# Kernel optimization log

Measured on AMD Instinct MI355X. Metric: run time of the kernel, lower is better.

The kernel has to match this reference:

```python
import jax, jax.numpy as jnp
import numpy as np

B, F, D = 1024, 16, 64
P = F * (F - 1) // 2  # 120 field pairs


def setup_inputs() -> dict:
    key = jax.random.key(0)
    k1, k2, k3 = jax.random.split(key, 3)
    x = jax.random.normal(k1, (B, F, D), dtype=jnp.float32)
    # torch Linear weight layout: [out_features, in_features] = [D, D*D], one per pair
    W = jax.random.normal(k2, (P, D, D * D), dtype=jnp.float32) * (1.0 / np.sqrt(D * D))
    b = jax.random.normal(k3, (P, D), dtype=jnp.float32) * 0.01
    return {"x": x, "W": W, "b": b}


def reference(x, W, b):
    # x: [B, F, D]; W: [P, D, D*D]; b: [P, D]
    Bs, Fs, Ds = x.shape
    Ps = W.shape[0]
    ii, jj = np.triu_indices(Fs, k=1)  # pair order matches nested (i, j>i) loop
    xi = x[:, ii, :]  # [B, P, D] -> left vector of outer product
    xj = x[:, jj, :]  # [B, P, D] -> right vector
    # Flattened outer tmp[b, a*D + c] = xi[b,p,a] * xj[b,p,c];
    # Linear: out = tmp @ W^T + b. Reshape W to [P, D_out, a, c] and fuse,
    # never materializing the [B, P, D*D] outer-product tensor.
    W3 = W.reshape(Ps, Ds, Ds, Ds)
    out = jnp.einsum('bpa,bpc,pkac->bpk', xi, xj, W3) + b[None, :, :]
    return out  # [B, P, D]
```

## Files before the change

kernel.cpp:

```cpp
#include <hip/hip_runtime.h>
#include <stdint.h>
#include <stddef.h>

constexpr int NB = 1024;
constexpr int NF = 16;
constexpr int ND = 64;
constexpr int NP = 120;
constexpr int KD = ND * ND;
constexpr int OUT_STRIDE = NP * ND;

using floatx4 = __attribute__((ext_vector_type(4))) float;
using short8  = __attribute__((ext_vector_type(8))) short;
using uint4v  = __attribute__((ext_vector_type(4))) uint32_t;

constexpr int XI_STRIDE = 68;
constexpr int BT_STRIDE = 72;

__device__ __forceinline__ uint32_t pack_bf16(float f0, float f1) {
    uint32_t u0 = __float_as_uint(f0) + 0x8000u;
    uint32_t u1 = __float_as_uint(f1) + 0x8000u;
    return __builtin_amdgcn_perm(u1, u0, 0x07060302u);
}

__global__ __launch_bounds__(256, 2)
void outer_kernel(const float* __restrict__ x, const float* __restrict__ W,
                  const float* __restrict__ bias, float* __restrict__ out)
{
    __shared__ float    lds_xi[256 * XI_STRIDE];
    __shared__ uint16_t lds_bt[ND * BT_STRIDE];

    const int p  = blockIdx.x;
    const int b0 = blockIdx.y * 256;

    int icol = 0, rem = p;
    while (rem >= NF - 1 - icol) { rem -= NF - 1 - icol; ++icol; }
    const int jcol = icol + 1 + rem;

    const int t    = threadIdx.x;
    const int wave = t >> 6;
    const int lane = t & 63;
    const int r    = lane & 15;
    const int quad = lane >> 4;

    {
        const float* src = x + (size_t)(b0 + t) * (NF * ND) + icol * ND;
        float* dst = lds_xi + t * XI_STRIDE;
        #pragma unroll
        for (int c = 0; c < ND; c += 4)
            *(floatx4*)(dst + c) = *(const floatx4*)(src + c);
    }

    float xj[4][2][8];
    #pragma unroll
    for (int ms = 0; ms < 4; ++ms) {
        const float* srow = x + (size_t)(b0 + wave*64 + ms*16 + r) * (NF * ND)
                              + jcol * ND + quad * 8;
        #pragma unroll
        for (int ks = 0; ks < 2; ++ks) {
            floatx4 v0 = *(const floatx4*)(srow + ks * 32);
            floatx4 v1 = *(const floatx4*)(srow + ks * 32 + 4);
            xj[ms][ks][0] = v0.x; xj[ms][ks][1] = v0.y;
            xj[ms][ks][2] = v0.z; xj[ms][ks][3] = v0.w;
            xj[ms][ks][4] = v1.x; xj[ms][ks][5] = v1.y;
            xj[ms][ks][6] = v1.z; xj[ms][ks][7] = v1.w;
        }
    }

    const int n_st = t >> 2;
    const int c_st = (t & 3) * 16;
    const float* wsrc = W + ((size_t)p * ND + n_st) * KD + c_st;
    uint16_t* bdst = lds_bt + n_st * BT_STRIDE + c_st;

    floatx4 w0 = *(const floatx4*)(wsrc + 0);
    floatx4 w1 = *(const floatx4*)(wsrc + 4);
    floatx4 w2 = *(const floatx4*)(wsrc + 8);
    floatx4 w3 = *(const floatx4*)(wsrc + 12);

    floatx4 acc[4][4] = {};

    #pragma unroll 1
    for (int a = 0; a < ND; ++a) {
        uint4v q0 = (uint4v){ pack_bf16(w0.x, w0.y), pack_bf16(w0.z, w0.w),
                              pack_bf16(w1.x, w1.y), pack_bf16(w1.z, w1.w) };
        uint4v q1 = (uint4v){ pack_bf16(w2.x, w2.y), pack_bf16(w2.z, w2.w),
                              pack_bf16(w3.x, w3.y), pack_bf16(w3.z, w3.w) };
        *(uint4v*)(bdst)     = q0;
        *(uint4v*)(bdst + 8) = q1;
        __syncthreads();

        if (a + 1 < ND) {
            const float* wn = wsrc + (size_t)(a + 1) * ND;
            w0 = *(const floatx4*)(wn + 0);
            w1 = *(const floatx4*)(wn + 4);
            w2 = *(const floatx4*)(wn + 8);
            w3 = *(const floatx4*)(wn + 12);
        }

        float xis[4];
        #pragma unroll
        for (int ms = 0; ms < 4; ++ms)
            xis[ms] = lds_xi[(wave*64 + ms*16 + r) * XI_STRIDE + a];

        #pragma unroll
        for (int ks = 0; ks < 2; ++ks) {
            short8 bf[4];
            #pragma unroll
            for (int ns = 0; ns < 4; ++ns)
                bf[ns] = *(const short8*)&lds_bt[(ns*16 + r) * BT_STRIDE
                                                 + ks*32 + quad*8];
            #pragma unroll
            for (int ms = 0; ms < 4; ++ms) {
                union { short8 s; uint32_t u[4]; } af;
                #pragma unroll
                for (int jj = 0; jj < 4; ++jj)
                    af.u[jj] = pack_bf16(xis[ms] * xj[ms][ks][2*jj],
                                         xis[ms] * xj[ms][ks][2*jj + 1]);
                #pragma unroll
                for (int ns = 0; ns < 4; ++ns)
                    acc[ms][ns] = __builtin_amdgcn_mfma_f32_16x16x32_bf16(
                        af.s, bf[ns], acc[ms][ns], 0, 0, 0);
            }
        }
        __syncthreads();
    }

    #pragma unroll
    for (int ns = 0; ns < 4; ++ns) {
        const float bb = bias[p * ND + ns*16 + r];
        #pragma unroll
        for (int ms = 0; ms < 4; ++ms) {
            #pragma unroll
            for (int reg = 0; reg < 4; ++reg) {
                const int row = b0 + wave*64 + ms*16 + quad*4 + reg;
                out[(size_t)row * OUT_STRIDE + p * ND + ns*16 + r]
                    = acc[ms][ns][reg] + bb;
            }
        }
    }
}

extern "C" void kernel_launch(void* const* d_in, const int* in_sizes, int n_in,
                              void* d_out, int out_size, void* d_ws, size_t ws_size,
                              hipStream_t stream) {
    const float* x    = (const float*)d_in[0];
    const float* W    = (const float*)d_in[1];
    const float* bias = (const float*)d_in[2];
    float* out = (float*)d_out;

    dim3 grid(NP, NB / 256);
    outer_kernel<<<grid, 256, 0, stream>>>(x, W, bias, out);
}
```

Measured before the change: 230.2 us.

## Factor xi scaling out of MFMA and double-buffer weight tiles in LDS

The kernel now keeps a fixed bf16 A fragment built from xj and runs MFMA against each weight slice with a zero accumulator. It then scales the result rows by xi[a] on the VALU and adds them into the accumulators, so the per-iteration xi*xj multiply and repack of A fragments goes away. xi is stored transposed in LDS as bf16, and the weight slice LDS buffer is double-buffered, which removes one barrier per iteration and prefetches two slices ahead. The cost is 64 extra VALU FMAs per iteration plus bf16 rounding of xi, and the separate per-a accumulation changes the numerics.

After: 379.1 us. +64.7%, slower.

```diff
diff --git a/kernel.cpp b/kernel.cpp
--- a/kernel.cpp
+++ b/kernel.cpp
@@ -12,8 +12,9 @@
 using floatx4 = __attribute__((ext_vector_type(4))) float;
 using short8  = __attribute__((ext_vector_type(8))) short;
 using uint4v  = __attribute__((ext_vector_type(4))) uint32_t;
+using ushort4v = __attribute__((ext_vector_type(4))) uint16_t;
 
-constexpr int XI_STRIDE = 68;
+constexpr int XT_STRIDE = 264;
 constexpr int BT_STRIDE = 72;
 
 __device__ __forceinline__ uint32_t pack_bf16(float f0, float f1) {
@@ -22,12 +23,20 @@
     return __builtin_amdgcn_perm(u1, u0, 0x07060302u);
 }
 
+__device__ __forceinline__ uint16_t to_bf16(float f) {
+    return (uint16_t)((__float_as_uint(f) + 0x8000u) >> 16);
+}
+
+__device__ __forceinline__ float from_bf16(uint16_t u) {
+    return __uint_as_float(((uint32_t)u) << 16);
+}
+
 __global__ __launch_bounds__(256, 2)
 void outer_kernel(const float* __restrict__ x, const float* __restrict__ W,
                   const float* __restrict__ bias, float* __restrict__ out)
 {
-    __shared__ float    lds_xi[256 * XI_STRIDE];
-    __shared__ uint16_t lds_bt[ND * BT_STRIDE];
+    __shared__ uint16_t lds_xit[ND * XT_STRIDE];
+    __shared__ uint16_t lds_bt[2][ND * BT_STRIDE];
 
     const int p  = blockIdx.x;
     const int b0 = blockIdx.y * 256;
@@ -44,13 +53,17 @@
 
     {
         const float* src = x + (size_t)(b0 + t) * (NF * ND) + icol * ND;
-        float* dst = lds_xi + t * XI_STRIDE;
         #pragma unroll
-        for (int c = 0; c < ND; c += 4)
-            *(floatx4*)(dst + c) = *(const floatx4*)(src + c);
+        for (int c = 0; c < ND; c += 4) {
+            floatx4 v = *(const floatx4*)(src + c);
+            lds_xit[(c + 0) * XT_STRIDE + t] = to_bf16(v.x);
+            lds_xit[(c + 1) * XT_STRIDE + t] = to_bf16(v.y);
+            lds_xit[(c + 2) * XT_STRIDE + t] = to_bf16(v.z);
+            lds_xit[(c + 3) * XT_STRIDE + t] = to_bf16(v.w);
+        }
     }
 
-    float xj[4][2][8];
+    short8 afrag[4][2];
     #pragma unroll
     for (int ms = 0; ms < 4; ++ms) {
         const float* srow = x + (size_t)(b0 + wave*64 + ms*16 + r) * (NF * ND)
@@ -59,68 +72,94 @@
         for (int ks = 0; ks < 2; ++ks) {
             floatx4 v0 = *(const floatx4*)(srow + ks * 32);
             floatx4 v1 = *(const floatx4*)(srow + ks * 32 + 4);
-            xj[ms][ks][0] = v0.x; xj[ms][ks][1] = v0.y;
-            xj[ms][ks][2] = v0.z; xj[ms][ks][3] = v0.w;
-            xj[ms][ks][4] = v1.x; xj[ms][ks][5] = v1.y;
-            xj[ms][ks][6] = v1.z; xj[ms][ks][7] = v1.w;
+            union { short8 s; uint32_t u[4]; } af;
+            af.u[0] = pack_bf16(v0.x, v0.y);
+            af.u[1] = pack_bf16(v0.z, v0.w);
+            af.u[2] = pack_bf16(v1.x, v1.y);
+            af.u[3] = pack_bf16(v1.z, v1.w);
+            afrag[ms][ks] = af.s;
         }
     }
 
     const int n_st = t >> 2;
     const int c_st = (t & 3) * 16;
     const float* wsrc = W + ((size_t)p * ND + n_st) * KD + c_st;
-    uint16_t* bdst = lds_bt + n_st * BT_STRIDE + c_st;
+    uint16_t* bdst0 = &lds_bt[0][n_st * BT_STRIDE + c_st];
+    uint16_t* bdst1 = &lds_bt[1][n_st * BT_STRIDE + c_st];
 
-    floatx4 w0 = *(const floatx4*)(wsrc + 0);
-    floatx4 w1 = *(const floatx4*)(wsrc + 4);
-    floatx4 w2 = *(const floatx4*)(wsrc + 8);
-    floatx4 w3 = *(const floatx4*)(wsrc + 12);
+    floatx4 wreg[2][4];
+
+    #pragma unroll
+    for (int q = 0; q < 4; ++q) wreg[0][q] = *(const floatx4*)(wsrc + q * 4);
+    {
+        uint4v q0 = (uint4v){ pack_bf16(wreg[0][0].x, wreg[0][0].y), pack_bf16(wreg[0][0].z, wreg[0][0].w),
+                              pack_bf16(wreg[0][1].x, wreg[0][1].y), pack_bf16(wreg[0][1].z, wreg[0][1].w) };
+        uint4v q1 = (uint4v){ pack_bf16(wreg[0][2].x, wreg[0][2].y), pack_bf16(wreg[0][2].z, wreg[0][2].w),
+                              pack_bf16(wreg[0][3].x, wreg[0][3].y), pack_bf16(wreg[0][3].z, wreg[0][3].w) };
+        *(uint4v*)(bdst0)     = q0;
+        *(uint4v*)(bdst0 + 8) = q1;
+    }
+    #pragma unroll
+    for (int q = 0; q < 4; ++q) wreg[1][q] = *(const floatx4*)(wsrc + ND + q * 4);
+    __syncthreads();
 
     floatx4 acc[4][4] = {};
+    const floatx4 zerof = (floatx4){0.f, 0.f, 0.f, 0.f};
 
-    #pragma unroll 1
+    #pragma unroll 2
     for (int a = 0; a < ND; ++a) {
-        uint4v q0 = (uint4v){ pack_bf16(w0.x, w0.y), pack_bf16(w0.z, w0.w),
-                              pack_bf16(w1.x, w1.y), pack_bf16(w1.z, w1.w) };
-        uint4v q1 = (uint4v){ pack_bf16(w2.x, w2.y), pack_bf16(w2.z, w2.w),
-                              pack_bf16(w3.x, w3.y), pack_bf16(w3.z, w3.w) };
-        *(uint4v*)(bdst)     = q0;
-        *(uint4v*)(bdst + 8) = q1;
-        __syncthreads();
+        const int cur = a & 1;
+
+        if (a + 2 < ND) {
+            const float* wn = wsrc + (size_t)(a + 2) * ND;
+            #pragma unroll
+            for (int q = 0; q < 4; ++q) wreg[cur][q] = *(const floatx4*)(wn + q * 4);
+        }
+
+        short8 bf[4][2];
+        #pragma unroll
+        for (int ns = 0; ns < 4; ++ns)
+            #pragma unroll
+            for (int ks = 0; ks < 2; ++ks)
+                bf[ns][ks] = *(const short8*)&lds_bt[cur][(ns*16 + r) * BT_STRIDE
+                                                          + ks*32 + quad*8];
+
+        float xiv[4][4];
+        #pragma unroll
+        for (int ms = 0; ms < 4; ++ms) {
+            ushort4v xv = *(const ushort4v*)&lds_xit[a * XT_STRIDE
+                                                     + wave*64 + ms*16 + quad*4];
+            xiv[ms][0] = from_bf16(xv.x);
+            xiv[ms][1] = from_bf16(xv.y);
+            xiv[ms][2] = from_bf16(xv.z);
+            xiv[ms][3] = from_bf16(xv.w);
+        }
+
+        #pragma unroll
+        for (int ms = 0; ms < 4; ++ms) {
+            #pragma unroll
+            for (int ns = 0; ns < 4; ++ns) {
+                floatx4 tacc = __builtin_amdgcn_mfma_f32_16x16x32_bf16(
+                    afrag[ms][0], bf[ns][0], zerof, 0, 0, 0);
+                tacc = __builtin_amdgcn_mfma_f32_16x16x32_bf16(
+                    afrag[ms][1], bf[ns][1], tacc, 0, 0, 0);
+                #pragma unroll
+                for (int reg = 0; reg < 4; ++reg)
+                    acc[ms][ns][reg] += xiv[ms][reg] * tacc[reg];
+            }
+        }
 
         if (a + 1 < ND) {
-            const float* wn = wsrc + (size_t)(a + 1) * ND;
-            w0 = *(const floatx4*)(wn + 0);
-            w1 = *(const floatx4*)(wn + 4);
-            w2 = *(const floatx4*)(wn + 8);
-            w3 = *(const floatx4*)(wn + 12);
+            const floatx4* wr = wreg[1 - cur];
+            uint4v q0 = (uint4v){ pack_bf16(wr[0].x, wr[0].y), pack_bf16(wr[0].z, wr[0].w),
+                                  pack_bf16(wr[1].x, wr[1].y), pack_bf16(wr[1].z, wr[1].w) };
+            uint4v q1 = (uint4v){ pack_bf16(wr[2].x, wr[2].y), pack_bf16(wr[2].z, wr[2].w),
+                                  pack_bf16(wr[3].x, wr[3].y), pack_bf16(wr[3].z, wr[3].w) };
+            uint16_t* bd = (cur ? bdst0 : bdst1);
+            *(uint4v*)(bd)     = q0;
+            *(uint4v*)(bd + 8) = q1;
         }
 
-        float xis[4];
-        #pragma unroll
-        for (int ms = 0; ms < 4; ++ms)
-            xis[ms] = lds_xi[(wave*64 + ms*16 + r) * XI_STRIDE + a];
-
-        #pragma unroll
-        for (int ks = 0; ks < 2; ++ks) {
-            short8 bf[4];
-            #pragma unroll
-            for (int ns = 0; ns < 4; ++ns)
-                bf[ns] = *(const short8*)&lds_bt[(ns*16 + r) * BT_STRIDE
-                                                 + ks*32 + quad*8];
-            #pragma unroll
-            for (int ms = 0; ms < 4; ++ms) {
-                union { short8 s; uint32_t u[4]; } af;
-                #pragma unroll
-                for (int jj = 0; jj < 4; ++jj)
-                    af.u[jj] = pack_bf16(xis[ms] * xj[ms][ks][2*jj],
-                                         xis[ms] * xj[ms][ks][2*jj + 1]);
-                #pragma unroll
-                for (int ns = 0; ns < 4; ++ns)
-                    acc[ms][ns] = __builtin_amdgcn_mfma_f32_16x16x32_bf16(
-                        af.s, bf[ns], acc[ms][ns], 0, 0, 0);
-            }
-        }
         __syncthreads();
     }
 
```
